# Optimization experiments

Hardware: AMD Instinct MI355X
Metric: run time of the kernel (lower is better)

The kernel has to match this reference:

```python
import jax, jax.numpy as jnp
import numpy as np
from jax.ops import segment_sum, segment_max

N, E, B = 100000, 400000, 2048
F_NODE, F_EDGE, G_DIM = 7, 3, 10
HID, H, C, L, T = 128, 4, 32, 4, 5
EPS = 1e-5
NEG_SLOPE = 0.2

def setup_inputs():
    key = jax.random.key(0)
    ks = iter(jax.random.split(key, 64))
    def nrm(shape, fan_in):
        return jax.random.normal(next(ks), shape, jnp.float32) / np.float32(np.sqrt(fan_in))
    return {
        "x": jax.random.normal(next(ks), (N, F_NODE), jnp.float32),
        "edge_index": jax.random.randint(next(ks), (2, E), 0, N),
        "edge_attr": jax.random.normal(next(ks), (E, F_EDGE), jnp.float32),
        "batch": jnp.sort(jax.random.randint(next(ks), (N,), 0, B)),
        "global_features": jax.random.normal(next(ks), (B, G_DIM), jnp.float32),
        "node_w": nrm((F_NODE, HID), F_NODE), "node_b": jnp.zeros((HID,), jnp.float32),
        "edge_w": nrm((F_EDGE, HID), F_EDGE), "edge_b": jnp.zeros((HID,), jnp.float32),
        "gat_lin_w": nrm((L, HID, H * C), HID),
        "gat_edge_w": nrm((L, HID, H * C), HID),
        "att_src": nrm((L, H, C), C), "att_dst": nrm((L, H, C), C), "att_edge": nrm((L, H, C), C),
        "gat_bias": jnp.zeros((L, H * C), jnp.float32),
        "bn_gamma": jnp.ones((L, HID), jnp.float32), "bn_beta": jnp.zeros((L, HID), jnp.float32),
        "bn_mean": jnp.zeros((L, HID), jnp.float32), "bn_var": jnp.ones((L, HID), jnp.float32),
        "gc_w": nrm((3 * HID, HID), 3 * HID), "gc_b": jnp.zeros((HID,), jnp.float32),
        "gf1_w": nrm((G_DIM, HID // 2), G_DIM), "gf1_b": jnp.zeros((HID // 2,), jnp.float32),
        "gf2_w": nrm((HID // 2, HID // 2), HID // 2), "gf2_b": jnp.zeros((HID // 2,), jnp.float32),
        "p1_w": nrm((HID + HID // 2, HID), HID + HID // 2), "p1_b": jnp.zeros((HID,), jnp.float32),
        "p2_w": nrm((HID, HID // 2), HID), "p2_b": jnp.zeros((HID // 2,), jnp.float32),
        "p3_w": nrm((HID // 2, T), HID // 2), "p3_b": jnp.zeros((T,), jnp.float32),
    }

def _forward(x, edge_attr, global_features,
             node_w, node_b, edge_w, edge_b,
             gat_lin_w, gat_edge_w, att_src, att_dst, att_edge, gat_bias,
             bn_gamma, bn_beta, bn_mean, bn_var,
             gc_w, gc_b, gf1_w, gf1_b, gf2_w, gf2_b,
             p1_w, p1_b, p2_w, p2_b, p3_w, p3_b,
             edge_index, batch):
    n = x.shape[0]
    b = global_features.shape[0]
    src, dst = edge_index[0], edge_index[1]
    loop = jnp.arange(n)

    h = x @ node_w + node_b                       # [N, HID]
    e = edge_attr @ edge_w + edge_b               # [E, HID]

    # PyG add_self_loops with fill_value='mean': self-loop edge feature is the
    # mean of incoming edge features (0 for isolated nodes).
    deg = segment_sum(jnp.ones((src.shape[0],), h.dtype), dst, num_segments=n)
    e_loop = segment_sum(e, dst, num_segments=n) / jnp.maximum(deg, 1.0)[:, None]
    fsrc = jnp.concatenate([src, loop])
    fdst = jnp.concatenate([dst, loop])
    fe = jnp.concatenate([e, e_loop], axis=0)     # [E+N, HID]

    for i in range(L):
        h_res = h
        xh = (h @ gat_lin_w[i]).reshape(n, H, C)
        eh = (fe @ gat_edge_w[i]).reshape(-1, H, C)
        a_s = jnp.einsum('nhc,hc->nh', xh, att_src[i])
        a_d = jnp.einsum('nhc,hc->nh', xh, att_dst[i])
        a_e = jnp.einsum('ehc,hc->eh', eh, att_edge[i])
        alpha = jax.nn.leaky_relu(a_s[fsrc] + a_d[fdst] + a_e, NEG_SLOPE)  # [E+N, H]
        # segment softmax over destination neighborhoods (self loops => nonempty)
        amax = segment_max(alpha, fdst, num_segments=n)
        expa = jnp.exp(alpha - amax[fdst])
        denom = segment_sum(expa, fdst, num_segments=n)
        coef = expa / denom[fdst]
        out = segment_sum(xh[fsrc] * coef[..., None], fdst, num_segments=n)
        out = out.reshape(n, H * C) + gat_bias[i]
        # BatchNorm (eval-mode running stats)
        out = (out - bn_mean[i]) * (bn_gamma[i] / jnp.sqrt(bn_var[i] + EPS)) + bn_beta[i]
        h = jax.nn.relu(out) + h_res

    # multi-pool readout
    cnt = segment_sum(jnp.ones((n,), h.dtype), batch, num_segments=b)
    gsum = segment_sum(h, batch, num_segments=b)
    gmean = gsum / jnp.maximum(cnt, 1.0)[:, None]
    gmax = segment_max(h, batch, num_segments=b)
    gmax = jnp.where(cnt[:, None] > 0, gmax, 0.0)
    graph = jnp.concatenate([gmean, gmax, gsum], axis=1)   # [B, 3*HID]
    graph = jax.nn.relu(graph @ gc_w + gc_b)
    glob = jax.nn.relu(global_features @ gf1_w + gf1_b) @ gf2_w + gf2_b
    comb = jnp.concatenate([graph, glob], axis=1)          # [B, HID + HID//2]
    hid = jax.nn.relu(comb @ p1_w + p1_b)
    hid = jax.nn.relu(hid @ p2_w + p2_b)
    return hid @ p3_w + p3_b                               # [B, T]

def reference(x, edge_index, edge_attr, batch, global_features,
              node_w, node_b, edge_w, edge_b,
              gat_lin_w, gat_edge_w, att_src, att_dst, att_edge, gat_bias,
              bn_gamma, bn_beta, bn_mean, bn_var,
              gc_w, gc_b, gf1_w, gf1_b, gf2_w, gf2_b,
              p1_w, p1_b, p2_w, p2_b, p3_w, p3_b):
    return _forward(x, edge_attr, global_features,
                    node_w, node_b, edge_w, edge_b,
                    gat_lin_w, gat_edge_w, att_src, att_dst, att_edge, gat_bias,
                    bn_gamma, bn_beta, bn_mean, bn_var,
                    gc_w, gc_b, gf1_w, gf1_b, gf2_w, gf2_b,
                    p1_w, p1_b, p2_w, p2_b, p3_w, p3_b,
                    edge_index, batch)
```

## Files before the change

### kernel.cpp

```cpp
#include <hip/hip_runtime.h>

#define N_NODES 100000
#define N_EDGES 400000
#define N_GRAPHS 2048
#define HID 128
#define NLAYER 4
#define TOUT 5
#define EPSV 1e-5f
#define SLOPE 0.2f
#define NB 98
#define GEMM_BLOCKS 782

typedef float v4f __attribute__((ext_vector_type(4)));
typedef __bf16 v8bf __attribute__((ext_vector_type(8)));

static __device__ __forceinline__ unsigned short f2bf_bits(float f){
  unsigned u = __builtin_bit_cast(unsigned, f);
  unsigned r = u + 0x7fffu + ((u >> 16) & 1u);
  return (unsigned short)(r >> 16);
}
static __device__ __forceinline__ float bfbits2f(unsigned short s){
  unsigned u = ((unsigned)s) << 16;
  return __builtin_bit_cast(float, u);
}
static __device__ __forceinline__ float bflo(unsigned u){
  return __builtin_bit_cast(float, u << 16);
}
static __device__ __forceinline__ float bfhi(unsigned u){
  return __builtin_bit_cast(float, u & 0xffff0000u);
}
static __device__ __forceinline__ float lrelu(float v){
  return v>0.f ? v : SLOPE*v;
}


__global__ void k_setup(const float* __restrict__ gat_edge_w, const float* __restrict__ att_edge,
                        const float* __restrict__ edge_w, const float* __restrict__ edge_b,
                        const float* __restrict__ gat_bias, const float* __restrict__ gamma,
                        const float* __restrict__ beta, const float* __restrict__ mean,
                        const float* __restrict__ var, const float* __restrict__ gat_lin_w,
                        const float* __restrict__ att_src, const float* __restrict__ att_dst,
                        const float* __restrict__ x, const float* __restrict__ nw,
                        const float* __restrict__ nb, unsigned* __restrict__ h16,
                        float* __restrict__ mebuf, float* __restrict__ bnA, float* __restrict__ bnS,
                        unsigned short* __restrict__ whiE, unsigned short* __restrict__ wloE,
                        unsigned short* __restrict__ whi,
                        int* __restrict__ deg, int* __restrict__ fill){
  int bid = blockIdx.x, t = threadIdx.x;
  if(bid < 16){
    int wv = t>>6, lane = t&63;
    int o = bid*4 + wv;
    int li = (o<48)? (o&15) : (o-48);
    int f = o>>4;
    int l = li>>2, hh = li&3;
    int c = lane&31, kk = lane>>5;
    float at_c = att_edge[l*128 + hh*32 + c];
    float acc = 0.f;
    #pragma unroll 8
    for(int t2=0; t2<64; ++t2){
      int k = kk*64 + t2;
      float wk = (o<48)? edge_w[f*128+k] : edge_b[k];
      acc += wk * gat_edge_w[l*16384 + k*128 + hh*32 + c];
    }
    acc *= at_c;
    acc += __shfl_xor(acc,1); acc += __shfl_xor(acc,2); acc += __shfl_xor(acc,4);
    acc += __shfl_xor(acc,8); acc += __shfl_xor(acc,16); acc += __shfl_xor(acc,32);
    if(lane==0) mebuf[o] = acc;
  } else if(bid == 16){
    for(int i=t; i<NLAYER*HID; i+=256){
      int l_ = i>>7, pos = i&127, lane = pos>>2, j = pos&3;
      int ch = ((lane>>3)<<5) + ((lane&7)<<1) + ((j&1)<<4) + (j>>1);
      int src = l_*128 + ch;
      float A = gamma[src]*rsqrtf(var[src]+EPSV);
      bnA[i] = A;
      bnS[i] = (gat_bias[src]-mean[src])*A + beta[src];
    }
  } else if(bid <= 1040){
    int wave = t>>6, lane = t&63;
    int i = (bid-17)*8 + wave*2 + (lane>>5);
    int l_ = i>>11, rest = i&2047, kp = rest>>4, col = rest&15;
    int sub = lane&31;
    float val = 0.f;
    if(col < 8){
      int h_ = col&3, isdst = col>>2;
      int ch = ((kp>>5)<<5) + ((kp&1)<<4) + ((kp&31)>>1);
      const float* at = (isdst? att_dst : att_src);
      val = gat_lin_w[l_*16384 + ch*128 + h_*32 + sub] * at[l_*128 + h_*32 + sub];
    }
    val += __shfl_xor(val,1); val += __shfl_xor(val,2); val += __shfl_xor(val,4);
    val += __shfl_xor(val,8); val += __shfl_xor(val,16);
    if(sub == 0){
      unsigned short hi = f2bf_bits(val);
      unsigned short lo = f2bf_bits(val - bfbits2f(hi));
      int kb=kp>>5, quad=(kp>>3)&3, jj=kp&7, lane2=quad*16+col;
      int dst = ((l_*4+kb)*64 + lane2)*8 + jj;
      whiE[dst]=hi; wloE[dst]=lo;
    }
  } else if(bid <= 1296){
    int tg = (bid-1041)*256 + t;
    int base = tg>>9, off = tg&511;
    int l = base>>5, kb=(base>>3)&3, cg=base&7;
    int lane = off>>3, j = off&7;
    int quad = lane>>4, r = lane&15;
    int kp = kb*32 + quad*8 + j;
    int k = ((kp>>5)<<5) | ((kp&1)<<4) | ((kp&31)>>1);
    whi[tg] = f2bf_bits(gat_lin_w[l*16384 + k*128 + cg*16 + r]);
  } else if(bid <= 1687){
    int tg = (bid-1297)*256 + t;
    if(tg < N_NODES){ deg[tg]=0; fill[tg]=0; }
  } else {
    int node = (bid-1688)*4 + (t>>6);
    int c = t&63;
    int ch = ((c>>4)<<5) + (c&15);
    float a0 = nb[ch], a1 = nb[ch+16];
    #pragma unroll
    for(int f=0; f<7; ++f){
      float xv = x[node*7+f];
      a0 += xv*nw[f*HID+ch];
      a1 += xv*nw[f*HID+ch+16];
    }
    unsigned p = (unsigned)f2bf_bits(a0) | ((unsigned)f2bf_bits(a1)<<16);
    h16[(size_t)node*64 + c] = p;
  }
}

__global__ void k_deg(const int* __restrict__ ei, int* __restrict__ deg){
  int e = blockIdx.x*256 + threadIdx.x;
  if(e < N_EDGES) atomicAdd(&deg[ei[N_EDGES+e]], 1);
}

__global__ void k_scan1(const int* __restrict__ deg, int* __restrict__ part){
  __shared__ int s[256];
  int t=threadIdx.x; int base = blockIdx.x*1024 + t*4;
  int sum=0;
  #pragma unroll
  for(int j=0;j<4;++j){ int i=base+j; sum += (i<N_NODES)? deg[i]:0; }
  s[t]=sum; __syncthreads();
  for(int off=128; off>0; off>>=1){ if(t<off) s[t]+=s[t+off]; __syncthreads(); }
  if(t==0) part[blockIdx.x]=s[0];
}
__global__ void k_scan3(const int* __restrict__ deg, const int* __restrict__ part,
                        int* __restrict__ rowptr){
  __shared__ int s[256];
  int t=threadIdx.x, b=blockIdx.x;
  int g = 0, tot = 0;
  for(int i=0;i<NB;++i){ int v = part[i]; g += (i<b)? v : 0; tot += v; }
  if(b==0 && t==0) rowptr[N_NODES]=tot;
  int base = b*1024 + t*4;
  int v[4]; int sum=0; int pre[4];
  #pragma unroll
  for(int j=0;j<4;++j){ int i=base+j; v[j]=(i<N_NODES)?deg[i]:0; pre[j]=sum; sum+=v[j]; }
  s[t]=sum; __syncthreads();
  for(int off=1; off<256; off<<=1){
    int xv = (t>=off)? s[t-off]:0; __syncthreads();
    s[t]+=xv; __syncthreads();
  }
  int toff = (t>0)? s[t-1]:0;
  #pragma unroll
  for(int j=0;j<4;++j){ int i=base+j; if(i<N_NODES) rowptr[i]=g+toff+pre[j]; }
}

__global__ void k_gemm(const unsigned short* __restrict__ h16,
                       const unsigned short* __restrict__ whi,
                       const unsigned short* __restrict__ whiE,
                       const unsigned short* __restrict__ wloE,
                       unsigned* __restrict__ xhb, float* __restrict__ as_, float* __restrict__ ad_,
                       const int* __restrict__ ei, const float* __restrict__ ea,
                       const int* __restrict__ rowptr, int* __restrict__ fill,
                       int* __restrict__ csr_src, float* __restrict__ ea_csr){
  if(blockIdx.x >= GEMM_BLOCKS){
    int e = (blockIdx.x - GEMM_BLOCKS)*256 + threadIdx.x;
    if(e < N_EDGES){
      int dst = ei[N_EDGES+e];
      int pos = rowptr[dst] + atomicAdd(&fill[dst],1);
      csr_src[pos] = ei[e];
      v4f q = {ea[e*3], ea[e*3+1], ea[e*3+2], 0.f};
      ((v4f*)ea_csr)[pos] = q;
    }
    return;
  }
  __shared__ unsigned sxh[4][2][16*68];
  int wave = threadIdx.x>>6, lane = threadIdx.x&63;
  int base = blockIdx.x*128;
  int q = lane>>4, r = lane&15;
  int r0[2];
  r0[0] = base + wave*16;
  r0[1] = base + 64 + wave*16;
  if(r0[0] > N_NODES-16) r0[0] = N_NODES-16;
  if(r0[1] > N_NODES-16) r0[1] = N_NODES-16;
  v8bf av[2][4];
  #pragma unroll
  for(int tt=0;tt<2;++tt){
    const unsigned short* hrow = h16 + (size_t)(r0[tt] + r)*HID;
    #pragma unroll
    for(int kb=0;kb<4;++kb)
      av[tt][kb] = *(const v8bf*)(hrow + kb*32 + q*8);
  }
  v4f acc[2][8];
  #pragma unroll
  for(int cg=0;cg<8;++cg){
    v4f a0 = {0.f,0.f,0.f,0.f}, a1 = {0.f,0.f,0.f,0.f};
    #pragma unroll
    for(int kb=0;kb<4;++kb){
      v8bf bhi = *(const v8bf*)(whi + ((kb*8+cg)*64 + lane)*8);
      a0 = __builtin_amdgcn_mfma_f32_16x16x32_bf16(av[0][kb], bhi, a0, 0,0,0);
      a1 = __builtin_amdgcn_mfma_f32_16x16x32_bf16(av[1][kb], bhi, a1, 0,0,0);
    }
    acc[0][cg]=a0; acc[1][cg]=a1;
  }
  v4f acc8[2] = {{0.f,0.f,0.f,0.f},{0.f,0.f,0.f,0.f}};
  #pragma unroll
  for(int kb=0;kb<4;++kb){
    v8bf bhi = *(const v8bf*)(whiE + (kb*64 + lane)*8);
    v8bf blo = *(const v8bf*)(wloE + (kb*64 + lane)*8);
    #pragma unroll
    for(int tt=0;tt<2;++tt){
      acc8[tt] = __builtin_amdgcn_mfma_f32_16x16x32_bf16(av[tt][kb], blo, acc8[tt], 0,0,0);
      acc8[tt] = __builtin_amdgcn_mfma_f32_16x16x32_bf16(av[tt][kb], bhi, acc8[tt], 0,0,0);
    }
  }
  #pragma unroll
  for(int tt=0;tt<2;++tt){
    #pragma unroll
    for(int m=0;m<4;++m){
      #pragma unroll
      for(int reg=0;reg<4;++reg){
        unsigned pack = (unsigned)f2bf_bits(acc[tt][2*m][reg]) | ((unsigned)f2bf_bits(acc[tt][2*m+1][reg])<<16);
        sxh[wave][tt][(q*4+reg)*68 + m*16 + r] = pack;
      }
    }
  }
  __syncthreads();
  {
    int rr = lane>>4, c4 = lane&15;
    #pragma unroll
    for(int tt=0;tt<2;++tt){
      #pragma unroll
      for(int rg=0; rg<4; ++rg){
        int i = rg*4 + rr;
        uint4 v = *(const uint4*)&sxh[wave][tt][i*68 + c4*4];
        *(uint4*)(xhb + (size_t)(r0[tt] + i)*64 + c4*4) = v;
      }
    }
  }
  #pragma unroll
  for(int tt=0;tt<2;++tt){
    if(r < 4){
      #pragma unroll
      for(int reg=0;reg<4;++reg)
        as_[(size_t)(r0[tt] + q*4 + reg)*4 + r] = acc8[tt][reg];
    } else if(r < 8){
      #pragma unroll
      for(int reg=0;reg<4;++reg)
        ad_[(size_t)(r0[tt] + q*4 + reg)*4 + (r-4)] = acc8[tt][reg];
    }
  }
}

__global__ void k_aggr(const unsigned* __restrict__ xhb, const float* __restrict__ as_,
    const float* __restrict__ ad_, const float* __restrict__ ea_csr,
    const float* __restrict__ mebuf,
    const int* __restrict__ rowptr, const int* __restrict__ csr_src,
    const float* __restrict__ bnA_l, const float* __restrict__ bnS_l,
    unsigned* __restrict__ h16, int layer){
  __shared__ float lds_coef[8][16*4];
  __shared__ int   lds_src[8][16];
  int hw = threadIdx.x>>5, lh = threadIdx.x&31;
  int lane = threadIdx.x&63;
  int node = blockIdx.x*8 + hw;
  if(node >= N_NODES) return;
  int s = rowptr[node], e = rowptr[node+1];
  int deg = e - s;
  int hh2 = lh>>3;
  const uint2* xrow = (const uint2*)xhb;
  float a0,a1,a2,a3;

  if(deg <= 16){
    int eidx = lh>>2, h = lh&3;
    int li = layer*4+h;
    float mec0=mebuf[li], mec1=mebuf[16+li], mec2=mebuf[32+li], meb=mebuf[48+li];
    float ad_h = ad_[node*4+h];
    int j0 = eidx;
    float t0 = 0.f, g0 = 0.f;
    int s0 = node;
    bool v0 = (j0 < deg);
    if(v0){
      s0 = csr_src[s+j0];
      v4f qq = ((const v4f*)ea_csr)[s+j0];
      t0 = qq.x*mec0 + qq.y*mec1 + qq.z*mec2;
      g0 = lrelu(as_[s0*4+h] + ad_h + t0 + meb);
    }
    float ts, ds, inv;
    if(deg <= 8){
      ts = t0;
      ts += __shfl_xor(ts,4); ts += __shfl_xor(ts,8); ts += __shfl_xor(ts,16);
      float lt = (deg>0) ? ts/(float)deg + meb : 0.f;
      float al = lrelu(as_[node*4+h] + ad_h + lt);
      float e0 = v0 ? __expf(g0-al) : 0.f;
      ds = e0;
      ds += __shfl_xor(ds,4); ds += __shfl_xor(ds,8); ds += __shfl_xor(ds,16);
      inv = 1.f/(ds+1.f);
      if(h==0) lds_src[hw][j0] = s0;
      lds_coef[hw][j0*4+h] = e0*inv;
    } else {
      int j1 = 8+eidx;
      float t1 = 0.f, g1 = 0.f;
      int s1 = node;
      bool v1 = (j1 < deg);
      if(v1){
        s1 = csr_src[s+j1];
        v4f qq = ((const v4f*)ea_csr)[s+j1];
        t1 = qq.x*mec0 + qq.y*mec1 + qq.z*mec2;
        g1 = lrelu(as_[s1*4+h] + ad_h + t1 + meb);
      }
      ts = t0+t1;
      ts += __shfl_xor(ts,4); ts += __shfl_xor(ts,8); ts += __shfl_xor(ts,16);
      float lt = ts/(float)deg + meb;
      float al = lrelu(as_[node*4+h] + ad_h + lt);
      float e0 = v0 ? __expf(g0-al) : 0.f;
      float e1 = v1 ? __expf(g1-al) : 0.f;
      ds = e0+e1;
      ds += __shfl_xor(ds,4); ds += __shfl_xor(ds,8); ds += __shfl_xor(ds,16);
      inv = 1.f/(ds+1.f);
      if(h==0){ lds_src[hw][j0]=s0; lds_src[hw][j1]=s1; }
      lds_coef[hw][j0*4+h] = e0*inv;
      lds_coef[hw][j1*4+h] = e1*inv;
    }
    float cs4 = __shfl(inv, (lane&32) | hh2);
    uint2 su = xrow[(size_t)node*32 + lh];
    int pdeg = (deg+1)&~1;
    a0=a1=a2=a3=0.f;
    for(int j=0;j<pdeg;j+=2){
      float ca = lds_coef[hw][j*4+hh2];
      float cb = lds_coef[hw][(j+1)*4+hh2];
      int sa = lds_src[hw][j], sb = lds_src[hw][j+1];
      uint2 ua = xrow[(size_t)sa*32+lh];
      uint2 ub = xrow[(size_t)sb*32+lh];
      a0 += ca*bflo(ua.x) + cb*bflo(ub.x);
      a1 += ca*bfhi(ua.x) + cb*bfhi(ub.x);
      a2 += ca*bflo(ua.y) + cb*bflo(ub.y);
      a3 += ca*bfhi(ua.y) + cb*bfhi(ub.y);
    }
    a0 += cs4*bflo(su.x); a1 += cs4*bfhi(su.x);
    a2 += cs4*bflo(su.y); a3 += cs4*bfhi(su.y);
  } else {
    int li = layer*4+hh2;
    float mec0=mebuf[li], mec1=mebuf[16+li], mec2=mebuf[32+li], meb=mebuf[48+li];
    float adv = ad_[node*4+hh2];
    float ts = 0.f;
    for(int j=s;j<e;++j){
      v4f qq = ((const v4f*)ea_csr)[j];
      ts += qq.x*mec0 + qq.y*mec1 + qq.z*mec2;
    }
    float al = lrelu(as_[node*4+hh2] + adv + ts/(float)deg + meb);
    float m = al, d = 1.f;
    uint2 su = xrow[(size_t)node*32 + lh];
    float c0=bflo(su.x),c1=bfhi(su.x),c2=bflo(su.y),c3=bfhi(su.y);
    for(int j=s;j<e;++j){
      int sr = csr_src[j];
      v4f qq = ((const v4f*)ea_csr)[j];
      float b = lrelu(as_[sr*4+hh2] + adv + qq.x*mec0+qq.y*mec1+qq.z*mec2+meb);
      uint2 uv = xrow[(size_t)sr*32 + lh];
      float nm = fmaxf(m,b);
      float sc = __expf(m-nm), eb = __expf(b-nm);
      d = d*sc + eb;
      c0 = c0*sc + eb*bflo(uv.x); c1 = c1*sc + eb*bfhi(uv.x);
      c2 = c2*sc + eb*bflo(uv.y); c3 = c3*sc + eb*bfhi(uv.y);
      m = nm;
    }
    float inv2 = 1.f/d;
    a0=c0*inv2; a1=c1*inv2; a2=c2*inv2; a3=c3*inv2;
  }

  {
    const v4f* A4 = (const v4f*)bnA_l;
    const v4f* S4 = (const v4f*)bnS_l;
    v4f A = A4[lh], S = S4[lh];
    uint2 hr = ((const uint2*)h16)[(size_t)node*32 + lh];
    float o0 = fmaxf(a0*A.x+S.x, 0.f) + bflo(hr.x);
    float o1 = fmaxf(a1*A.y+S.y, 0.f) + bfhi(hr.x);
    float o2 = fmaxf(a2*A.z+S.z, 0.f) + bflo(hr.y);
    float o3 = fmaxf(a3*A.w+S.w, 0.f) + bfhi(hr.y);
    uint2 p;
    p.x = (unsigned)f2bf_bits(o0) | ((unsigned)f2bf_bits(o1)<<16);
    p.y = (unsigned)f2bf_bits(o2) | ((unsigned)f2bf_bits(o3)<<16);
    ((uint2*)h16)[(size_t)node*32 + lh] = p;
  }
}

__global__ void k_tail(const unsigned* __restrict__ h16, const int* __restrict__ batch,
   const float* __restrict__ gf,
   const float* __restrict__ gc_w, const float* __restrict__ gc_b,
   const float* __restrict__ gf1_w, const float* __restrict__ gf1_b,
   const float* __restrict__ gf2_w, const float* __restrict__ gf2_b,
   const float* __restrict__ p1_w, const float* __restrict__ p1_b,
   const float* __restrict__ p2_w, const float* __restrict__ p2_b,
   const float* __restrict__ p3_w, const float* __restrict__ p3_b,
   float* __restrict__ out){
  __shared__ float sgtT[384*12];
  __shared__ v4f   redA[256];
  __shared__ v4f   redB[256];
  __shared__ float hid1s[8*64];
  __shared__ float combT[192*12];
  __shared__ float partialb[8*128];
  __shared__ float r1T[128*12];
  __shared__ float ppb[3*8*64];
  __shared__ float r2T[64*12];
  __shared__ int   sbv[9];

  int t = threadIdx.x;
  int g0 = blockIdx.x*8;

  if(t < 9){
    int target = g0 + t;
    int lo=0, hi=N_NODES;
    while(lo<hi){ int mid=(lo+hi)>>1; if(batch[mid] < target) lo=mid+1; else hi=mid; }
    sbv[t]=lo;
  }
  __syncthreads();

  {
    int w2 = t&31;
    int j8 = t>>5;
    const uint2* xr = (const uint2*)h16;
    for(int g=0; g<8; ++g){
      int s=sbv[g], e=sbv[g+1];
      float sl0=0.f,sh0=0.f,sl1=0.f,sh1=0.f;
      float ml0=-3.4e38f, mh0=-3.4e38f, ml1=-3.4e38f, mh1=-3.4e38f;
      for(int i=s+j8; i<e; i+=8){
        uint2 v = xr[(size_t)i*32 + w2];
        float a=bflo(v.x), b=bfhi(v.x), c=bflo(v.y), d=bfhi(v.y);
        sl0+=a; sh0+=b; sl1+=c; sh1+=d;
        ml0=fmaxf(ml0,a); mh0=fmaxf(mh0,b); ml1=fmaxf(ml1,c); mh1=fmaxf(mh1,d);
      }
      redA[t] = (v4f){sl0,sh0,sl1,sh1};
      redB[t] = (v4f){ml0,mh0,ml1,mh1};
      __syncthreads();
      if(t < 32){
        v4f S = redA[t], M = redB[t];
        #pragma unroll
        for(int jj=1; jj<8; ++jj){
          v4f a2 = redA[jj*32+t], b2 = redB[jj*32+t];
          S.x+=a2.x; S.y+=a2.y; S.z+=a2.z; S.w+=a2.w;
          M.x=fmaxf(M.x,b2.x); M.y=fmaxf(M.y,b2.y);
          M.z=fmaxf(M.z,b2.z); M.w=fmaxf(M.w,b2.w);
        }
        int cnt = sbv[g+1]-sbv[g];
        float invc = 1.f/(float)(cnt>1?cnt:1);
        if(cnt==0){ M.x=0.f; M.y=0.f; M.z=0.f; M.w=0.f; }
        int bb = w2>>3, rr = (w2&7)*2;
        int c00 = bb*32+rr, c01=c00+16, c10=c00+1, c11=c00+17;
        sgtT[c00*12+g]=S.x*invc; sgtT[c01*12+g]=S.y*invc;
        sgtT[c10*12+g]=S.z*invc; sgtT[c11*12+g]=S.w*invc;
        sgtT[(128+c00)*12+g]=M.x; sgtT[(128+c01)*12+g]=M.y;
        sgtT[(128+c10)*12+g]=M.z; sgtT[(128+c11)*12+g]=M.w;
        sgtT[(256+c00)*12+g]=S.x; sgtT[(256+c01)*12+g]=S.y;
        sgtT[(256+c10)*12+g]=S.z; sgtT[(256+c11)*12+g]=S.w;
      }
      __syncthreads();
    }
  }

  {
    int c=t&63, gg=t>>6;
    #pragma unroll
    for(int p=0;p<2;++p){
      int g = p*4+gg;
      float a = gf1_b[c];
      #pragma unroll
      for(int i=0;i<10;++i) a += gf[(size_t)(g0+g)*10+i]*gf1_w[i*64+c];
      hid1s[g*64+c] = fmaxf(a,0.f);
    }
  }

  int c = t&127, half = t>>7;
  float acc[8];
  #pragma unroll
  for(int g=0;g<8;++g) acc[g]=0.f;
  {
    int kb = half*192;
    for(int kk=0; kk<192; ++kk){
      int k = kb+kk;
      float wv = gc_w[k*128+c];
      v4f s0v = *(const v4f*)&sgtT[k*12];
      v4f s1v = *(const v4f*)&sgtT[k*12+4];
      acc[0]+=s0v.x*wv; acc[1]+=s0v.y*wv; acc[2]+=s0v.z*wv; acc[3]+=s0v.w*wv;
      acc[4]+=s1v.x*wv; acc[5]+=s1v.y*wv; acc[6]+=s1v.z*wv; acc[7]+=s1v.w*wv;
    }
  }
  __syncthreads();

  {
    int cc=t&63, gg=t>>6;
    #pragma unroll
    for(int p=0;p<2;++p){
      int g = p*4+gg;
      float a = gf2_b[cc];
      for(int k=0;k<64;++k) a += hid1s[g*64+k]*gf2_w[k*64+cc];
      combT[(128+cc)*12+g] = a;
    }
  }
  if(half==1){
    #pragma unroll
    for(int g=0;g<8;++g) partialb[g*128+c]=acc[g];
  }
  __syncthreads();
  if(half==0){
    float bias = gc_b[c];
    #pragma unroll
    for(int g=0;g<8;++g)
      combT[c*12+g] = fmaxf(acc[g]+partialb[g*128+c]+bias, 0.f);
  }
  __syncthreads();

  float a1[8];
  #pragma unroll
  for(int g=0;g<8;++g) a1[g]=0.f;
  {
    int kb = half*96;
    for(int kk=0; kk<96; ++kk){
      int k = kb+kk;
      float wv = p1_w[k*128+c];
      v4f s0v = *(const v4f*)&combT[k*12];
      v4f s1v = *(const v4f*)&combT[k*12+4];
      a1[0]+=s0v.x*wv; a1[1]+=s0v.y*wv; a1[2]+=s0v.z*wv; a1[3]+=s0v.w*wv;
      a1[4]+=s1v.x*wv; a1[5]+=s1v.y*wv; a1[6]+=s1v.z*wv; a1[7]+=s1v.w*wv;
    }
  }
  if(half==1){
    #pragma unroll
    for(int g=0;g<8;++g) partialb[g*128+c]=a1[g];
  }
  __syncthreads();
  if(half==0){
    float b1 = p1_b[c];
    #pragma unroll
    for(int g=0;g<8;++g)
      r1T[c*12+g] = fmaxf(a1[g]+partialb[g*128+c]+b1, 0.f);
  }
  __syncthreads();

  {
    int c2=t&63, qd=t>>6;
    float a2[8];
    #pragma unroll
    for(int g=0;g<8;++g) a2[g]=0.f;
    int kb = qd*32;
    for(int kk=0; kk<32; ++kk){
      int k = kb+kk;
      float wv = p2_w[k*64+c2];
      v4f s0v = *(const v4f*)&r1T[k*12];
      v4f s1v = *(const v4f*)&r1T[k*12+4];
      a2[0]+=s0v.x*wv; a2[1]+=s0v.y*wv; a2[2]+=s0v.z*wv; a2[3]+=s0v.w*wv;
      a2[4]+=s1v.x*wv; a2[5]+=s1v.y*wv; a2[6]+=s1v.z*wv; a2[7]+=s1v.w*wv;
    }
    if(qd>0){
      #pragma unroll
      for(int g=0;g<8;++g) ppb[((qd-1)*8+g)*64+c2]=a2[g];
    }
    __syncthreads();
    if(qd==0){
      float b2 = p2_b[c2];
      #pragma unroll
      for(int g=0;g<8;++g){
        float v = a2[g] + ppb[g*64+c2] + ppb[(8+g)*64+c2] + ppb[(16+g)*64+c2] + b2;
        r2T[c2*12+g] = fmaxf(v,0.f);
      }
    }
    __syncthreads();
  }

  if(t < 40){
    int g = t/5, o = t%5;
    float a = p3_b[o];
    for(int k=0;k<64;++k) a += r2T[k*12+g]*p3_w[k*TOUT+o];
    out[(size_t)(g0+g)*TOUT+o] = a;
  }
}

extern "C" void kernel_launch(void* const* d_in, const int* in_sizes, int n_in,
                              void* d_out, int out_size, void* d_ws, size_t ws_size,
                              hipStream_t stream){
  (void)in_sizes; (void)n_in; (void)out_size; (void)ws_size;
  const float* x        = (const float*)d_in[0];
  const int*   ei       = (const int*)d_in[1];
  const float* ea       = (const float*)d_in[2];
  const int*   batch    = (const int*)d_in[3];
  const float* gfin     = (const float*)d_in[4];
  const float* node_w   = (const float*)d_in[5];
  const float* node_b   = (const float*)d_in[6];
  const float* edge_w   = (const float*)d_in[7];
  const float* edge_b   = (const float*)d_in[8];
  const float* gat_lin_w  = (const float*)d_in[9];
  const float* gat_edge_w = (const float*)d_in[10];
  const float* att_src  = (const float*)d_in[11];
  const float* att_dst  = (const float*)d_in[12];
  const float* att_edge = (const float*)d_in[13];
  const float* gat_bias = (const float*)d_in[14];
  const float* bn_gamma = (const float*)d_in[15];
  const float* bn_beta  = (const float*)d_in[16];
  const float* bn_mean  = (const float*)d_in[17];
  const float* bn_var   = (const float*)d_in[18];
  const float* gc_w = (const float*)d_in[19];
  const float* gc_b = (const float*)d_in[20];
  const float* gf1_w = (const float*)d_in[21];
  const float* gf1_b = (const float*)d_in[22];
  const float* gf2_w = (const float*)d_in[23];
  const float* gf2_b = (const float*)d_in[24];
  const float* p1_w = (const float*)d_in[25];
  const float* p1_b = (const float*)d_in[26];
  const float* p2_w = (const float*)d_in[27];
  const float* p2_b = (const float*)d_in[28];
  const float* p3_w = (const float*)d_in[29];
  const float* p3_b = (const float*)d_in[30];
  float* out = (float*)d_out;

  char* w = (char*)d_ws;
  size_t o = 0;
  auto carve = [&](size_t bytes)->char*{
    char* p = w + o; o += (bytes + 255) & ~(size_t)255; return p;
  };
  unsigned* xhb = (unsigned*)carve((size_t)N_NODES*64*4);
  unsigned* h16 = (unsigned*)carve((size_t)N_NODES*64*4);
  float* ea_csr = (float*)carve((size_t)N_EDGES*4*4);
  float* as_    = (float*)carve((size_t)N_NODES*4*4);
  float* ad_    = (float*)carve((size_t)N_NODES*4*4);
  int* deg      = (int*)carve((size_t)N_NODES*4);
  int* rowptr   = (int*)carve((size_t)(N_NODES+1)*4);
  int* fill     = (int*)carve((size_t)N_NODES*4);
  int* csr_src  = (int*)carve((size_t)N_EDGES*4);
  int* part     = (int*)carve(1024*4);
  float* mebuf  = (float*)carve(64*4);
  float* bnA    = (float*)carve((size_t)NLAYER*HID*4);
  float* bnS    = (float*)carve((size_t)NLAYER*HID*4);
  unsigned short* whi = (unsigned short*)carve(65536*2);
  unsigned short* whiE = (unsigned short*)carve(8192*2);
  unsigned short* wloE = (unsigned short*)carve(8192*2);

  k_setup<<<1688 + N_NODES/4, 256, 0, stream>>>(gat_edge_w, att_edge, edge_w, edge_b,
        gat_bias, bn_gamma, bn_beta, bn_mean, bn_var,
        gat_lin_w, att_src, att_dst, x, node_w, node_b, h16,
        mebuf, bnA, bnS, whiE, wloE, whi, deg, fill);
  k_deg<<<(N_EDGES+255)/256, 256, 0, stream>>>(ei, deg);
  k_scan1<<<NB,256,0,stream>>>(deg, part);
  k_scan3<<<NB,256,0,stream>>>(deg, part, rowptr);

  for(int l=0;l<NLAYER;++l){
    int gb = (l==0) ? GEMM_BLOCKS + (N_EDGES+255)/256 : GEMM_BLOCKS;
    k_gemm<<<gb,256,0,stream>>>((const unsigned short*)h16,
        whi + l*16384, whiE + l*2048, wloE + l*2048,
        xhb, as_, ad_, ei, ea, rowptr, fill, csr_src, ea_csr);
    k_aggr<<<(N_NODES+7)/8,256,0,stream>>>(xhb, as_, ad_, ea_csr, mebuf,
        rowptr, csr_src, bnA + l*128, bnS + l*128, h16, l);
  }

  k_tail<<<N_GRAPHS/8,256,0,stream>>>(h16, batch, gfin, gc_w, gc_b, gf1_w, gf1_b,
        gf2_w, gf2_b, p1_w, p1_b, p2_w, p2_b, p3_w, p3_b, out);
}
```

Baseline: 432.8 us.

## Split tail into per-graph pooling kernel and 4-graph MLP head kernel

The fused tail kernel, which pooled 8 graphs serially per block with many barriers and then ran the MLP head, is replaced by two kernels. A pooling kernel runs one block per graph (2048 blocks) and writes mean/max/sum to a global buffer. A head kernel processes 4 graphs per block with vectorized v4f accumulation and 4-way unrolled weight loads. This exposes far more parallelism in the pooling stage, at the cost of an extra launch and a global round trip for the pooled features, plus more weight reloads in the head.

```diff
diff --git a/kernel.cpp b/kernel.cpp
--- a/kernel.cpp
+++ b/kernel.cpp
@@ -12,6 +12,7 @@
 #define GEMM_BLOCKS 782
 
 typedef float v4f __attribute__((ext_vector_type(4)));
+typedef float v2f __attribute__((ext_vector_type(2)));
 typedef __bf16 v8bf __attribute__((ext_vector_type(8)));
 
 static __device__ __forceinline__ unsigned short f2bf_bits(float f){
@@ -388,7 +389,57 @@
   }
 }
 
-__global__ void k_tail(const unsigned* __restrict__ h16, const int* __restrict__ batch,
+__global__ void k_pool(const unsigned* __restrict__ h16, const int* __restrict__ batch,
+                       float* __restrict__ pool){
+  __shared__ v4f redA[256];
+  __shared__ v4f redB[256];
+  __shared__ int sbp[2];
+  int t = threadIdx.x, g = blockIdx.x;
+  if(t < 2){
+    int target = g + t;
+    int lo=0, hi=N_NODES;
+    while(lo<hi){ int mid=(lo+hi)>>1; if(batch[mid] < target) lo=mid+1; else hi=mid; }
+    sbp[t]=lo;
+  }
+  __syncthreads();
+  int s = sbp[0], e = sbp[1];
+  int w2 = t&31, j8 = t>>5;
+  const uint2* xr = (const uint2*)h16;
+  float sl0=0.f,sh0=0.f,sl1=0.f,sh1=0.f;
+  float ml0=-3.4e38f, mh0=-3.4e38f, ml1=-3.4e38f, mh1=-3.4e38f;
+  for(int i=s+j8; i<e; i+=8){
+    uint2 v = xr[(size_t)i*32 + w2];
+    float a=bflo(v.x), b=bfhi(v.x), c=bflo(v.y), d=bfhi(v.y);
+    sl0+=a; sh0+=b; sl1+=c; sh1+=d;
+    ml0=fmaxf(ml0,a); mh0=fmaxf(mh0,b); ml1=fmaxf(ml1,c); mh1=fmaxf(mh1,d);
+  }
+  redA[t] = (v4f){sl0,sh0,sl1,sh1};
+  redB[t] = (v4f){ml0,mh0,ml1,mh1};
+  __syncthreads();
+  if(t < 32){
+    v4f S = redA[t], M = redB[t];
+    #pragma unroll
+    for(int jj=1; jj<8; ++jj){
+      v4f a2 = redA[jj*32+t], b2 = redB[jj*32+t];
+      S.x+=a2.x; S.y+=a2.y; S.z+=a2.z; S.w+=a2.w;
+      M.x=fmaxf(M.x,b2.x); M.y=fmaxf(M.y,b2.y);
+      M.z=fmaxf(M.z,b2.z); M.w=fmaxf(M.w,b2.w);
+    }
+    int cnt = e-s;
+    float invc = 1.f/(float)(cnt>1?cnt:1);
+    if(cnt==0){ M.x=0.f; M.y=0.f; M.z=0.f; M.w=0.f; }
+    int c00 = (w2>>3)*32 + (w2&7)*2;
+    float* pg = pool + (size_t)g*384;
+    *(v2f*)&pg[c00]        = (v2f){S.x*invc, S.z*invc};
+    *(v2f*)&pg[c00+16]     = (v2f){S.y*invc, S.w*invc};
+    *(v2f*)&pg[128+c00]    = (v2f){M.x, M.z};
+    *(v2f*)&pg[128+c00+16] = (v2f){M.y, M.w};
+    *(v2f*)&pg[256+c00]    = (v2f){S.x, S.z};
+    *(v2f*)&pg[256+c00+16] = (v2f){S.y, S.w};
+  }
+}
+
+__global__ void k_head(const float* __restrict__ pool,
    const float* __restrict__ gf,
    const float* __restrict__ gc_w, const float* __restrict__ gc_b,
    const float* __restrict__ gf1_w, const float* __restrict__ gf1_b,
@@ -397,183 +448,128 @@
    const float* __restrict__ p2_w, const float* __restrict__ p2_b,
    const float* __restrict__ p3_w, const float* __restrict__ p3_b,
    float* __restrict__ out){
-  __shared__ float sgtT[384*12];
-  __shared__ v4f   redA[256];
-  __shared__ v4f   redB[256];
-  __shared__ float hid1s[8*64];
-  __shared__ float combT[192*12];
-  __shared__ float partialb[8*128];
-  __shared__ float r1T[128*12];
-  __shared__ float ppb[3*8*64];
-  __shared__ float r2T[64*12];
-  __shared__ int   sbv[9];
-
+  __shared__ float poolT[384*4];
+  __shared__ float hid1s[64*4];
+  __shared__ float partial[128*4];
+  __shared__ float combT[192*4];
+  __shared__ float r1T[128*4];
+  __shared__ float ppb[3*64*4];
+  __shared__ float r2T[64*4];
   int t = threadIdx.x;
-  int g0 = blockIdx.x*8;
-
-  if(t < 9){
-    int target = g0 + t;
-    int lo=0, hi=N_NODES;
-    while(lo<hi){ int mid=(lo+hi)>>1; if(batch[mid] < target) lo=mid+1; else hi=mid; }
-    sbv[t]=lo;
-  }
-  __syncthreads();
-
+  int g0 = blockIdx.x*4;
+
+  for(int idx=t; idx<1536; idx+=256)
+    poolT[idx] = pool[(size_t)(g0+(idx&3))*384 + (idx>>2)];
   {
-    int w2 = t&31;
-    int j8 = t>>5;
-    const uint2* xr = (const uint2*)h16;
-    for(int g=0; g<8; ++g){
-      int s=sbv[g], e=sbv[g+1];
-      float sl0=0.f,sh0=0.f,sl1=0.f,sh1=0.f;
-      float ml0=-3.4e38f, mh0=-3.4e38f, ml1=-3.4e38f, mh1=-3.4e38f;
-      for(int i=s+j8; i<e; i+=8){
-        uint2 v = xr[(size_t)i*32 + w2];
-        float a=bflo(v.x), b=bfhi(v.x), c=bflo(v.y), d=bfhi(v.y);
-        sl0+=a; sh0+=b; sl1+=c; sh1+=d;
-        ml0=fmaxf(ml0,a); mh0=fmaxf(mh0,b); ml1=fmaxf(ml1,c); mh1=fmaxf(mh1,d);
-      }
-      redA[t] = (v4f){sl0,sh0,sl1,sh1};
-      redB[t] = (v4f){ml0,mh0,ml1,mh1};
-      __syncthreads();
-      if(t < 32){
-        v4f S = redA[t], M = redB[t];
-        #pragma unroll
-        for(int jj=1; jj<8; ++jj){
-          v4f a2 = redA[jj*32+t], b2 = redB[jj*32+t];
-          S.x+=a2.x; S.y+=a2.y; S.z+=a2.z; S.w+=a2.w;
-          M.x=fmaxf(M.x,b2.x); M.y=fmaxf(M.y,b2.y);
-          M.z=fmaxf(M.z,b2.z); M.w=fmaxf(M.w,b2.w);
-        }
-        int cnt = sbv[g+1]-sbv[g];
-        float invc = 1.f/(float)(cnt>1?cnt:1);
-        if(cnt==0){ M.x=0.f; M.y=0.f; M.z=0.f; M.w=0.f; }
-        int bb = w2>>3, rr = (w2&7)*2;
-        int c00 = bb*32+rr, c01=c00+16, c10=c00+1, c11=c00+17;
-        sgtT[c00*12+g]=S.x*invc; sgtT[c01*12+g]=S.y*invc;
-        sgtT[c10*12+g]=S.z*invc; sgtT[c11*12+g]=S.w*invc;
-        sgtT[(128+c00)*12+g]=M.x; sgtT[(128+c01)*12+g]=M.y;
-        sgtT[(128+c10)*12+g]=M.z; sgtT[(128+c11)*12+g]=M.w;
-        sgtT[(256+c00)*12+g]=S.x; sgtT[(256+c01)*12+g]=S.y;
-        sgtT[(256+c10)*12+g]=S.z; sgtT[(256+c11)*12+g]=S.w;
-      }
-      __syncthreads();
-    }
-  }
-
-  {
-    int c=t&63, gg=t>>6;
-    #pragma unroll
-    for(int p=0;p<2;++p){
-      int g = p*4+gg;
-      float a = gf1_b[c];
-      #pragma unroll
-      for(int i=0;i<10;++i) a += gf[(size_t)(g0+g)*10+i]*gf1_w[i*64+c];
-      hid1s[g*64+c] = fmaxf(a,0.f);
-    }
-  }
+    int c=t&63, g=t>>6;
+    float a = gf1_b[c];
+    #pragma unroll
+    for(int i=0;i<10;++i) a += gf[(size_t)(g0+g)*10+i]*gf1_w[i*64+c];
+    hid1s[c*4+g] = fmaxf(a,0.f);
+  }
+  __syncthreads();
 
   int c = t&127, half = t>>7;
-  float acc[8];
-  #pragma unroll
-  for(int g=0;g<8;++g) acc[g]=0.f;
+  const v4f* poolv = (const v4f*)poolT;
+  const v4f* combv = (const v4f*)combT;
+  const v4f* r1v = (const v4f*)r1T;
+
+  v4f acc = {0.f,0.f,0.f,0.f};
   {
     int kb = half*192;
-    for(int kk=0; kk<192; ++kk){
+    for(int kk=0; kk<192; kk+=4){
       int k = kb+kk;
-      float wv = gc_w[k*128+c];
-      v4f s0v = *(const v4f*)&sgtT[k*12];
-      v4f s1v = *(const v4f*)&sgtT[k*12+4];
-      acc[0]+=s0v.x*wv; acc[1]+=s0v.y*wv; acc[2]+=s0v.z*wv; acc[3]+=s0v.w*wv;
-      acc[4]+=s1v.x*wv; acc[5]+=s1v.y*wv; acc[6]+=s1v.z*wv; acc[7]+=s1v.w*wv;
-    }
-  }
-  __syncthreads();
-
+      float w0 = gc_w[(k+0)*128+c];
+      float w1 = gc_w[(k+1)*128+c];
+      float w2 = gc_w[(k+2)*128+c];
+      float w3 = gc_w[(k+3)*128+c];
+      v4f p0=poolv[k+0], p1=poolv[k+1], p2=poolv[k+2], p3=poolv[k+3];
+      acc += p0*w0; acc += p1*w1; acc += p2*w2; acc += p3*w3;
+    }
+  }
   {
-    int cc=t&63, gg=t>>6;
-    #pragma unroll
-    for(int p=0;p<2;++p){
-      int g = p*4+gg;
-      float a = gf2_b[cc];
-      for(int k=0;k<64;++k) a += hid1s[g*64+k]*gf2_w[k*64+cc];
-      combT[(128+cc)*12+g] = a;
-    }
-  }
-  if(half==1){
-    #pragma unroll
-    for(int g=0;g<8;++g) partialb[g*128+c]=acc[g];
-  }
+    int cc=t&63, g=t>>6;
+    float a = gf2_b[cc];
+    #pragma unroll 4
+    for(int k=0;k<64;++k) a += hid1s[k*4+g]*gf2_w[k*64+cc];
+    combT[(128+cc)*4+g] = a;
+  }
+  if(half==1) *(v4f*)&partial[c*4] = acc;
   __syncthreads();
   if(half==0){
+    v4f pb = *(const v4f*)&partial[c*4];
     float bias = gc_b[c];
-    #pragma unroll
-    for(int g=0;g<8;++g)
-      combT[c*12+g] = fmaxf(acc[g]+partialb[g*128+c]+bias, 0.f);
-  }
-  __syncthreads();
-
-  float a1[8];
-  #pragma unroll
-  for(int g=0;g<8;++g) a1[g]=0.f;
+    v4f r;
+    r.x = fmaxf(acc.x+pb.x+bias, 0.f);
+    r.y = fmaxf(acc.y+pb.y+bias, 0.f);
+    r.z = fmaxf(acc.z+pb.z+bias, 0.f);
+    r.w = fmaxf(acc.w+pb.w+bias, 0.f);
+    *(v4f*)&combT[c*4] = r;
+  }
+  __syncthreads();
+
+  v4f a1 = {0.f,0.f,0.f,0.f};
   {
     int kb = half*96;
-    for(int kk=0; kk<96; ++kk){
+    for(int kk=0; kk<96; kk+=4){
       int k = kb+kk;
-      float wv = p1_w[k*128+c];
-      v4f s0v = *(const v4f*)&combT[k*12];
-      v4f s1v = *(const v4f*)&combT[k*12+4];
-      a1[0]+=s0v.x*wv; a1[1]+=s0v.y*wv; a1[2]+=s0v.z*wv; a1[3]+=s0v.w*wv;
-      a1[4]+=s1v.x*wv; a1[5]+=s1v.y*wv; a1[6]+=s1v.z*wv; a1[7]+=s1v.w*wv;
-    }
-  }
-  if(half==1){
-    #pragma unroll
-    for(int g=0;g<8;++g) partialb[g*128+c]=a1[g];
-  }
+      float w0 = p1_w[(k+0)*128+c];
+      float w1 = p1_w[(k+1)*128+c];
+      float w2 = p1_w[(k+2)*128+c];
+      float w3 = p1_w[(k+3)*128+c];
+      v4f p0=combv[k+0], p1=combv[k+1], p2=combv[k+2], p3=combv[k+3];
+      a1 += p0*w0; a1 += p1*w1; a1 += p2*w2; a1 += p3*w3;
+    }
+  }
+  if(half==1) *(v4f*)&partial[c*4] = a1;
   __syncthreads();
   if(half==0){
+    v4f pb = *(const v4f*)&partial[c*4];
     float b1 = p1_b[c];
-    #pragma unroll
-    for(int g=0;g<8;++g)
-      r1T[c*12+g] = fmaxf(a1[g]+partialb[g*128+c]+b1, 0.f);
+    v4f r;
+    r.x = fmaxf(a1.x+pb.x+b1, 0.f);
+    r.y = fmaxf(a1.y+pb.y+b1, 0.f);
+    r.z = fmaxf(a1.z+pb.z+b1, 0.f);
+    r.w = fmaxf(a1.w+pb.w+b1, 0.f);
+    *(v4f*)&r1T[c*4] = r;
   }
   __syncthreads();
 
   {
     int c2=t&63, qd=t>>6;
-    float a2[8];
-    #pragma unroll
-    for(int g=0;g<8;++g) a2[g]=0.f;
+    v4f a2 = {0.f,0.f,0.f,0.f};
     int kb = qd*32;
-    for(int kk=0; kk<32; ++kk){
+    for(int kk=0; kk<32; kk+=4){
       int k = kb+kk;
-      float wv = p2_w[k*64+c2];
-      v4f s0v = *(const v4f*)&r1T[k*12];
-      v4f s1v = *(const v4f*)&r1T[k*12+4];
-      a2[0]+=s0v.x*wv; a2[1]+=s0v.y*wv; a2[2]+=s0v.z*wv; a2[3]+=s0v.w*wv;
-      a2[4]+=s1v.x*wv; a2[5]+=s1v.y*wv; a2[6]+=s1v.z*wv; a2[7]+=s1v.w*wv;
-    }
-    if(qd>0){
-      #pragma unroll
-      for(int g=0;g<8;++g) ppb[((qd-1)*8+g)*64+c2]=a2[g];
-    }
+      float w0 = p2_w[(k+0)*64+c2];
+      float w1 = p2_w[(k+1)*64+c2];
+      float w2 = p2_w[(k+2)*64+c2];
+      float w3 = p2_w[(k+3)*64+c2];
+      v4f p0=r1v[k+0], p1=r1v[k+1], p2=r1v[k+2], p3=r1v[k+3];
+      a2 += p0*w0; a2 += p1*w1; a2 += p2*w2; a2 += p3*w3;
+    }
+    if(qd>0) *(v4f*)&ppb[((qd-1)*64+c2)*4] = a2;
     __syncthreads();
     if(qd==0){
+      v4f q1 = *(const v4f*)&ppb[(0*64+c2)*4];
+      v4f q2 = *(const v4f*)&ppb[(1*64+c2)*4];
+      v4f q3 = *(const v4f*)&ppb[(2*64+c2)*4];
       float b2 = p2_b[c2];
-      #pragma unroll
-      for(int g=0;g<8;++g){
-        float v = a2[g] + ppb[g*64+c2] + ppb[(8+g)*64+c2] + ppb[(16+g)*64+c2] + b2;
-        r2T[c2*12+g] = fmaxf(v,0.f);
-      }
+      v4f r;
+      r.x = fmaxf(a2.x+q1.x+q2.x+q3.x+b2, 0.f);
+      r.y = fmaxf(a2.y+q1.y+q2.y+q3.y+b2, 0.f);
+      r.z = fmaxf(a2.z+q1.z+q2.z+q3.z+b2, 0.f);
+      r.w = fmaxf(a2.w+q1.w+q2.w+q3.w+b2, 0.f);
+      *(v4f*)&r2T[c2*4] = r;
     }
     __syncthreads();
   }
 
-  if(t < 40){
+  if(t < 20){
     int g = t/5, o = t%5;
     float a = p3_b[o];
-    for(int k=0;k<64;++k) a += r2T[k*12+g]*p3_w[k*TOUT+o];
+    #pragma unroll 4
+    for(int k=0;k<64;++k) a += r2T[k*4+g]*p3_w[k*TOUT+o];
     out[(size_t)(g0+g)*TOUT+o] = a;
   }
 }
@@ -636,6 +632,7 @@
   unsigned short* whi = (unsigned short*)carve(65536*2);
   unsigned short* whiE = (unsigned short*)carve(8192*2);
   unsigned short* wloE = (unsigned short*)carve(8192*2);
+  float* pool   = (float*)carve((size_t)N_GRAPHS*384*4);
 
   k_setup<<<1688 + N_NODES/4, 256, 0, stream>>>(gat_edge_w, att_edge, edge_w, edge_b,
         gat_bias, bn_gamma, bn_beta, bn_mean, bn_var,
@@ -654,6 +651,7 @@
         rowptr, csr_src, bnA + l*128, bnS + l*128, h16, l);
   }
 
-  k_tail<<<N_GRAPHS/8,256,0,stream>>>(h16, batch, gfin, gc_w, gc_b, gf1_w, gf1_b,
+  k_pool<<<N_GRAPHS,256,0,stream>>>(h16, batch, pool);
+  k_head<<<N_GRAPHS/4,256,0,stream>>>(pool, gfin, gc_w, gc_b, gf1_w, gf1_b,
         gf2_w, gf2_b, p1_w, p1_b, p2_w, p2_b, p3_w, p3_b, out);
 }
```

Result: faster. 422.9 us (-2.3%).
